# Kernel tuning notes

Hardware: AMD Instinct MI355X
Metric: run time of the kernel (lower is better)

Reference implementation:

```python
import jax, jax.numpy as jnp
import numpy as np

SMOOTH = 1.0

def setup_inputs() -> dict:
    key = jax.random.key(0)
    k1, k2 = jax.random.split(key)
    shape = (2, 4, 64, 256, 256)  # [B, organs, D, H, W]
    predict = jax.random.normal(k1, shape, dtype=jnp.float32)
    target = jax.random.uniform(k2, shape, dtype=jnp.float32)
    return {"predict": predict, "target": target}

def reference(predict, target):
    # sigmoid over whole prediction tensor (done once in DiceLoss.forward)
    p = jax.nn.sigmoid(predict)
    B, O, D = p.shape[0], p.shape[1], p.shape[2]
    # BinaryDiceLoss views each [D, H, W] organ slice as (D, H*W):
    pf = p.reshape(B, O, D, -1)
    tf = target.reshape(B, O, D, -1)
    num = jnp.sum(pf * tf, axis=-1)                      # [B, O, D]
    den = jnp.sum(pf, axis=-1) + jnp.sum(tf, axis=-1) + SMOOTH
    dice_loss = 1.0 - 2.0 * num / den                    # [B, O, D]
    # slices with first element == -1 are ignored
    valid = (tf[..., 0] != -1).astype(dice_loss.dtype)   # [B, O, D]
    per_slice_avg = jnp.sum(dice_loss * valid, axis=-1) / jnp.sum(valid, axis=-1)  # [B, O]
    # outer loop averages over all B*4 (b, organ) pairs
    return jnp.mean(per_slice_avg)
```

## Files before the change

kernel.cpp:

```cpp
#include <hip/hip_runtime.h>


constexpr int HW     = 256 * 256;
constexpr int NSLICE = 2 * 4 * 64;
constexpr int NPAIR  = 2 * 4;
constexpr int T      = 256;
constexpr int CHUNKS_PER_SLICE = 4;
constexpr int NCHUNK = NSLICE * CHUNKS_PER_SLICE;
constexpr int CHUNK_ELEMS = HW / CHUNKS_PER_SLICE;
constexpr int NITER  = CHUNK_ELEMS / 4 / T;
constexpr int BATCH  = 8;


__global__ __launch_bounds__(T) void dice_stage1(
    const float* __restrict__ predict,
    const float* __restrict__ target,
    float* __restrict__ ws)
{
    const int chunk = blockIdx.x;
    const int tid   = threadIdx.x;
    const size_t base = (size_t)chunk * CHUNK_ELEMS;
    const float4* __restrict__ p4 = (const float4*)(predict + base);
    const float4* __restrict__ t4 = (const float4*)(target + base);

    float s_pt0 = 0.f, s_pt1 = 0.f, s_p = 0.f, s_t = 0.f;

#pragma unroll
    for (int k0 = 0; k0 < NITER; k0 += BATCH) {
        float4 pv[BATCH], tv[BATCH];
#pragma unroll
        for (int j = 0; j < BATCH; ++j) {
            pv[j] = p4[(k0 + j) * T + tid];
            tv[j] = t4[(k0 + j) * T + tid];
        }
        __builtin_amdgcn_sched_barrier(0);
#pragma unroll
        for (int j = 0; j < BATCH; ++j) {
            float e0 = 1.f / (1.f + __expf(-pv[j].x));
            float e1 = 1.f / (1.f + __expf(-pv[j].y));
            float e2 = 1.f / (1.f + __expf(-pv[j].z));
            float e3 = 1.f / (1.f + __expf(-pv[j].w));
            s_pt0 += e0 * tv[j].x + e1 * tv[j].y;
            s_pt1 += e2 * tv[j].z + e3 * tv[j].w;
            s_p   += (e0 + e1) + (e2 + e3);
            s_t   += (tv[j].x + tv[j].y) + (tv[j].z + tv[j].w);
        }
    }

    float s_pt = s_pt0 + s_pt1;

#pragma unroll
    for (int off = 32; off > 0; off >>= 1) {
        s_pt += __shfl_down(s_pt, off, 64);
        s_p  += __shfl_down(s_p,  off, 64);
        s_t  += __shfl_down(s_t,  off, 64);
    }

    __shared__ float l_pt[T / 64], l_p[T / 64], l_t[T / 64];
    const int wave = tid >> 6;
    const int lane = tid & 63;
    if (lane == 0) { l_pt[wave] = s_pt; l_p[wave] = s_p; l_t[wave] = s_t; }
    __syncthreads();

    if (tid == 0) {
        float a = 0.f, b = 0.f, c = 0.f;
#pragma unroll
        for (int w = 0; w < T / 64; ++w) { a += l_pt[w]; b += l_p[w]; c += l_t[w]; }
        ws[chunk]              = a;
        ws[NCHUNK + chunk]     = b;
        ws[2 * NCHUNK + chunk] = c;
    }
}

__global__ __launch_bounds__(NSLICE) void dice_stage2(
    const float* __restrict__ ws,
    const float* __restrict__ target,
    float* __restrict__ out)
{
    const int s = threadIdx.x;
    float num = 0.f, sp = 0.f, st = 0.f;
#pragma unroll
    for (int c = 0; c < CHUNKS_PER_SLICE; ++c) {
        const int id = s * CHUNKS_PER_SLICE + c;
        num += ws[id];
        sp  += ws[NCHUNK + id];
        st  += ws[2 * NCHUNK + id];
    }
    float den   = sp + st + 1.0f;
    float dice  = 1.0f - 2.0f * num / den;
    float valid = (target[(size_t)s * HW] != -1.0f) ? 1.0f : 0.0f;

    float dv = dice * valid;
    float v  = valid;
#pragma unroll
    for (int off = 32; off > 0; off >>= 1) {
        dv += __shfl_down(dv, off, 64);
        v  += __shfl_down(v,  off, 64);
    }
    __shared__ float pair_avg[NPAIR];
    const int wave = s >> 6;
    const int lane = s & 63;
    if (lane == 0) pair_avg[wave] = dv / v;
    __syncthreads();
    if (s == 0) {
        float acc = 0.f;
#pragma unroll
        for (int w = 0; w < NPAIR; ++w) acc += pair_avg[w];
        out[0] = acc * (1.0f / NPAIR);
    }
}

extern "C" void kernel_launch(void* const* d_in, const int* in_sizes, int n_in,
                              void* d_out, int out_size, void* d_ws, size_t ws_size,
                              hipStream_t stream) {
    const float* predict = (const float*)d_in[0];
    const float* target  = (const float*)d_in[1];
    float* ws  = (float*)d_ws;
    float* out = (float*)d_out;

    dice_stage1<<<NCHUNK, T, 0, stream>>>(predict, target, ws);
    dice_stage2<<<1, NSLICE, 0, stream>>>(ws, target, out);
}
```

Before: 281.3 us.

## Process one float4 per thread and reduce slices via atomics

```diff
diff --git a/kernel.cpp b/kernel.cpp
--- a/kernel.cpp
+++ b/kernel.cpp
@@ -5,49 +5,32 @@
 constexpr int NSLICE = 2 * 4 * 64;
 constexpr int NPAIR  = 2 * 4;
 constexpr int T      = 256;
-constexpr int CHUNKS_PER_SLICE = 4;
-constexpr int NCHUNK = NSLICE * CHUNKS_PER_SLICE;
-constexpr int CHUNK_ELEMS = HW / CHUNKS_PER_SLICE;
-constexpr int NITER  = CHUNK_ELEMS / 4 / T;
-constexpr int BATCH  = 8;
+constexpr int NBLK   = NSLICE * HW / (T * 4);
+constexpr int BLOCKS_PER_SLICE = HW / (T * 4);
 
 
+__global__ __launch_bounds__(1024) void zero_ws(float* __restrict__ ws) {
+    const int i = blockIdx.x * 1024 + threadIdx.x;
+    if (i < 3 * NSLICE) ws[i] = 0.f;
+}
+
 __global__ __launch_bounds__(T) void dice_stage1(
-    const float* __restrict__ predict,
-    const float* __restrict__ target,
+    const float4* __restrict__ p4,
+    const float4* __restrict__ t4,
     float* __restrict__ ws)
 {
-    const int chunk = blockIdx.x;
-    const int tid   = threadIdx.x;
-    const size_t base = (size_t)chunk * CHUNK_ELEMS;
-    const float4* __restrict__ p4 = (const float4*)(predict + base);
-    const float4* __restrict__ t4 = (const float4*)(target + base);
+    const int idx = blockIdx.x * T + threadIdx.x;
+    const float4 pv = p4[idx];
+    const float4 tv = t4[idx];
 
-    float s_pt0 = 0.f, s_pt1 = 0.f, s_p = 0.f, s_t = 0.f;
+    const float e0 = 1.f / (1.f + __expf(-pv.x));
+    const float e1 = 1.f / (1.f + __expf(-pv.y));
+    const float e2 = 1.f / (1.f + __expf(-pv.z));
+    const float e3 = 1.f / (1.f + __expf(-pv.w));
 
-#pragma unroll
-    for (int k0 = 0; k0 < NITER; k0 += BATCH) {
-        float4 pv[BATCH], tv[BATCH];
-#pragma unroll
-        for (int j = 0; j < BATCH; ++j) {
-            pv[j] = p4[(k0 + j) * T + tid];
-            tv[j] = t4[(k0 + j) * T + tid];
-        }
-        __builtin_amdgcn_sched_barrier(0);
-#pragma unroll
-        for (int j = 0; j < BATCH; ++j) {
-            float e0 = 1.f / (1.f + __expf(-pv[j].x));
-            float e1 = 1.f / (1.f + __expf(-pv[j].y));
-            float e2 = 1.f / (1.f + __expf(-pv[j].z));
-            float e3 = 1.f / (1.f + __expf(-pv[j].w));
-            s_pt0 += e0 * tv[j].x + e1 * tv[j].y;
-            s_pt1 += e2 * tv[j].z + e3 * tv[j].w;
-            s_p   += (e0 + e1) + (e2 + e3);
-            s_t   += (tv[j].x + tv[j].y) + (tv[j].z + tv[j].w);
-        }
-    }
-
-    float s_pt = s_pt0 + s_pt1;
+    float s_pt = (e0 * tv.x + e1 * tv.y) + (e2 * tv.z + e3 * tv.w);
+    float s_p  = (e0 + e1) + (e2 + e3);
+    float s_t  = (tv.x + tv.y) + (tv.z + tv.w);
 
 #pragma unroll
     for (int off = 32; off > 0; off >>= 1) {
@@ -56,19 +39,18 @@
         s_t  += __shfl_down(s_t,  off, 64);
     }
 
-    __shared__ float l_pt[T / 64], l_p[T / 64], l_t[T / 64];
-    const int wave = tid >> 6;
-    const int lane = tid & 63;
-    if (lane == 0) { l_pt[wave] = s_pt; l_p[wave] = s_p; l_t[wave] = s_t; }
+    __shared__ float l[3][T / 64];
+    const int wave = threadIdx.x >> 6;
+    const int lane = threadIdx.x & 63;
+    if (lane == 0) { l[0][wave] = s_pt; l[1][wave] = s_p; l[2][wave] = s_t; }
     __syncthreads();
 
-    if (tid == 0) {
-        float a = 0.f, b = 0.f, c = 0.f;
+    if (threadIdx.x < 3) {
+        float v = 0.f;
 #pragma unroll
-        for (int w = 0; w < T / 64; ++w) { a += l_pt[w]; b += l_p[w]; c += l_t[w]; }
-        ws[chunk]              = a;
-        ws[NCHUNK + chunk]     = b;
-        ws[2 * NCHUNK + chunk] = c;
+        for (int w = 0; w < T / 64; ++w) v += l[threadIdx.x][w];
+        const int slice = blockIdx.x / BLOCKS_PER_SLICE;
+        atomicAdd(&ws[threadIdx.x * NSLICE + slice], v);
     }
 }
 
@@ -78,17 +60,10 @@
     float* __restrict__ out)
 {
     const int s = threadIdx.x;
-    float num = 0.f, sp = 0.f, st = 0.f;
-#pragma unroll
-    for (int c = 0; c < CHUNKS_PER_SLICE; ++c) {
-        const int id = s * CHUNKS_PER_SLICE + c;
-        num += ws[id];
-        sp  += ws[NCHUNK + id];
-        st  += ws[2 * NCHUNK + id];
-    }
-    float den   = sp + st + 1.0f;
-    float dice  = 1.0f - 2.0f * num / den;
-    float valid = (target[(size_t)s * HW] != -1.0f) ? 1.0f : 0.0f;
+    const float num = ws[s];
+    const float den = ws[NSLICE + s] + ws[2 * NSLICE + s] + 1.0f;
+    const float dice  = 1.0f - 2.0f * num / den;
+    const float valid = (target[(size_t)s * HW] != -1.0f) ? 1.0f : 0.0f;
 
     float dv = dice * valid;
     float v  = valid;
@@ -113,11 +88,13 @@
 extern "C" void kernel_launch(void* const* d_in, const int* in_sizes, int n_in,
                               void* d_out, int out_size, void* d_ws, size_t ws_size,
                               hipStream_t stream) {
-    const float* predict = (const float*)d_in[0];
-    const float* target  = (const float*)d_in[1];
+    const float4* predict = (const float4*)d_in[0];
+    const float4* target4 = (const float4*)d_in[1];
+    const float*  target  = (const float*)d_in[1];
     float* ws  = (float*)d_ws;
     float* out = (float*)d_out;
 
-    dice_stage1<<<NCHUNK, T, 0, stream>>>(predict, target, ws);
+    zero_ws    <<<2, 1024, 0, stream>>>(ws);
+    dice_stage1<<<NBLK, T, 0, stream>>>(predict, target4, ws);
     dice_stage2<<<1, NSLICE, 0, stream>>>(ws, target, out);
 }
```

After: 290.9 us. 1.03x slower.
